# Performance work log

Hardware: AMD Instinct MI355X
Metric: run time of the kernel (lower is better)

The kernel has to match this reference:

```python
import jax, jax.numpy as jnp
import numpy as np

N_NODES = 100000
N_EDGES = 1000000
D_FEAT = 64
N_ETYPES = 8
TEMPERATURE = 1.0
EPS = 1e-8


def setup_inputs() -> dict:
    key = jax.random.key(0)
    k1, k2, k3, k4, k5, k6, k7 = jax.random.split(key, 7)
    feat = jax.random.normal(k1, (N_NODES, D_FEAT), dtype=jnp.float32)
    # xavier_normal-ish scale for params (exact init values don't matter for correctness testing)
    attn = jax.random.normal(k2, (1, D_FEAT), dtype=jnp.float32) * 0.1
    edge_weight = jax.random.normal(k3, (N_ETYPES, N_ETYPES), dtype=jnp.float32) * 0.5
    edge_weight_param = jax.random.normal(k4, (N_ETYPES, 1), dtype=jnp.float32) * 0.5
    src = jax.random.randint(k5, (N_EDGES,), 0, N_NODES, dtype=jnp.int32)
    dst = jax.random.randint(k6, (N_EDGES,), 0, N_NODES, dtype=jnp.int32)
    # e_feat is 1-based edge type (indexed as e_feat - 1 in the original module)
    e_feat = jax.random.randint(k7, (N_EDGES,), 1, N_ETYPES + 1, dtype=jnp.int32)
    return {"feat": feat, "attn": attn, "edge_weight": edge_weight,
            "edge_weight_param": edge_weight_param, "src": src, "dst": dst,
            "e_feat": e_feat}


def reference(feat, attn, edge_weight, edge_weight_param, src, dst, e_feat):
    N = feat.shape[0]
    # node mask: 1 where node feature vector is non-zero, else 0
    node_abs = jnp.sum(jnp.abs(feat), axis=-1, keepdims=True)          # [N,1]
    node_mask = jnp.where(node_abs == 0, 0.0, 1.0).astype(feat.dtype)  # [N,1]
    # per-node attention logit (feats_type == 6)
    nw = jnp.sum(feat * attn, axis=-1, keepdims=True)                  # [N,1]
    # per-edge-type weight: edge_weight @ edge_weight_param + 1
    ew_table = edge_weight @ edge_weight_param + 1.0                   # [T,1]
    ew = ew_table[e_feat - 1]                                          # [E,1]
    nw_exp = jnp.exp(nw / TEMPERATURE) * node_mask                     # [N,1]
    # message pass 1: copy_src(nw_exp) -> sum at dst (normalizer)
    msg_w = nw_exp[src]                                                # [E,1]
    nw_exp_sum = jax.ops.segment_sum(msg_w, dst, num_segments=N)       # [N,1]
    # apply_edges copy_src + per-edge-type scaling
    ew = msg_w * ew                                                    # [E,1]
    # message pass 2: u_mul_e(ft, ew) -> sum at dst
    ft = jax.ops.segment_sum(feat[src] * ew, dst, num_segments=N)      # [N,D]
    denom = jnp.where(nw_exp_sum < EPS, 1.0, nw_exp_sum)
    rst = ft / denom
    # keep original features for non-masked (nonzero) nodes
    rst = rst * (1.0 - node_mask) + feat * node_mask
    return rst


if __name__ == "__main__":
    out = reference(**setup_inputs())
    print(out.shape, out.dtype)
```

## Files before the change

### kernel.cpp

```cpp
#include <hip/hip_runtime.h>
#include <hip/hip_bf16.h>
#include <math.h>

#define D_FEAT 64
#define N_ETYPES 8
#define EPS_F 1e-8f

__global__ void node_kernel(const float* __restrict__ feat,
                            const float* __restrict__ attn,
                            float* __restrict__ out,
                            float* __restrict__ nw_exp,
                            float* __restrict__ nw_exp_sum,
                            int* __restrict__ mask,
                            int N) {
    int gid  = blockIdx.x * blockDim.x + threadIdx.x;
    int node = gid >> 4;
    int sub  = gid & 15;
    if (node >= N) return;

    const float4 f = ((const float4*)feat)[(size_t)node * 16 + sub];
    const float4 a = ((const float4*)attn)[sub];

    ((float4*)out)[(size_t)node * 16 + sub] = f;

    float abss = fabsf(f.x) + fabsf(f.y) + fabsf(f.z) + fabsf(f.w);
    float dot  = f.x * a.x + f.y * a.y + f.z * a.z + f.w * a.w;

    #pragma unroll
    for (int off = 1; off < 16; off <<= 1) {
        abss += __shfl_xor(abss, off);
        dot  += __shfl_xor(dot,  off);
    }

    if (sub == 0) {
        int m = (abss == 0.0f) ? 0 : 1;
        mask[node]       = m;
        nw_exp[node]     = m ? expf(dot) : 0.0f;
        nw_exp_sum[node] = 0.0f;
    }
}

__global__ void edge_kernel(const int* __restrict__ src,
                            const int* __restrict__ dst,
                            const int* __restrict__ e_feat,
                            const float* __restrict__ feat,
                            const float* __restrict__ nw_exp,
                            const int* __restrict__ mask,
                            const float* __restrict__ edge_weight,
                            const float* __restrict__ edge_weight_param,
                            float* __restrict__ out,
                            float* __restrict__ nw_exp_sum,
                            int E) {
    int e = blockIdx.x * blockDim.x + threadIdx.x;
    if (e >= E) return;
    int d = dst[e];
    if (mask[d] != 0) return;
    int s = src[e];
    float w = nw_exp[s];
    atomicAdd(&nw_exp_sum[d], w);
    int t = e_feat[e] - 1;
    float ewv = 1.0f;
    #pragma unroll
    for (int j = 0; j < N_ETYPES; ++j)
        ewv += edge_weight[t * N_ETYPES + j] * edge_weight_param[j];
    float scale = w * ewv;
    const float* fs = feat + (size_t)s * D_FEAT;
    float*       od = out  + (size_t)d * D_FEAT;
    #pragma unroll 4
    for (int k = 0; k < D_FEAT; ++k)
        atomicAdd(&od[k], fs[k] * scale);
}

__global__ void fixup_kernel(float* __restrict__ out,
                             const float* __restrict__ nw_exp_sum,
                             const int* __restrict__ mask,
                             int N) {
    int n = blockIdx.x * blockDim.x + threadIdx.x;
    if (n >= N || mask[n] != 0) return;
    float s = nw_exp_sum[n];
    float denom = (s < EPS_F) ? 1.0f : s;
    float* row = out + (size_t)n * D_FEAT;
    #pragma unroll 4
    for (int k = 0; k < D_FEAT; ++k)
        row[k] = row[k] / denom;
}

extern "C" void kernel_launch(void* const* d_in, const int* in_sizes, int n_in,
                              void* d_out, int out_size, void* d_ws, size_t ws_size,
                              hipStream_t stream) {
    const float* feat              = (const float*)d_in[0];
    const float* attn              = (const float*)d_in[1];
    const float* edge_weight       = (const float*)d_in[2];
    const float* edge_weight_param = (const float*)d_in[3];
    const int*   src               = (const int*)d_in[4];
    const int*   dst               = (const int*)d_in[5];
    const int*   e_feat            = (const int*)d_in[6];
    float*       out               = (float*)d_out;

    const int N = in_sizes[0] / D_FEAT;
    const int E = in_sizes[4];

    float* nw_exp     = (float*)d_ws;
    float* nw_exp_sum = nw_exp + N;
    int*   mask       = (int*)(nw_exp_sum + N);

    const int threadsA = 256;
    const int nodesPerBlock = threadsA / 16;
    node_kernel<<<(N + nodesPerBlock - 1) / nodesPerBlock, threadsA, 0, stream>>>(
        feat, attn, out, nw_exp, nw_exp_sum, mask, N);

    edge_kernel<<<(E + 255) / 256, 256, 0, stream>>>(
        src, dst, e_feat, feat, nw_exp, mask, edge_weight, edge_weight_param,
        out, nw_exp_sum, E);

    fixup_kernel<<<(N + 255) / 256, 256, 0, stream>>>(
        out, nw_exp_sum, mask, N);
}
```

Measured before the change: 98.55 us.

## Skip edge and fixup passes when no node has an all-zero feature row

The node kernel now raises a device flag whenever it finds an all-zero feature row. The edge and fixup kernels check that flag and exit at once when no such node exists, so in that case the 1M-edge scan with its dst/mask gathers is avoided. Per-node exp weight, running sum and mask are packed into one float4 side record, and feat/out copies use nontemporal loads and stores. The edge and fixup kernels switch to fixed-size grid-stride launches. The flag is never zeroed on the host, so the kernels rely on the workspace not already holding 1; a stale 1 only causes unneeded work, not a wrong result.

```diff
diff --git a/kernel.cpp b/kernel.cpp
--- a/kernel.cpp
+++ b/kernel.cpp
@@ -6,22 +6,23 @@
 #define N_ETYPES 8
 #define EPS_F 1e-8f
 
+typedef float v4f __attribute__((ext_vector_type(4)));
+
 __global__ void node_kernel(const float* __restrict__ feat,
                             const float* __restrict__ attn,
                             float* __restrict__ out,
-                            float* __restrict__ nw_exp,
-                            float* __restrict__ nw_exp_sum,
-                            int* __restrict__ mask,
+                            v4f* __restrict__ side,
+                            int* __restrict__ flag,
                             int N) {
     int gid  = blockIdx.x * blockDim.x + threadIdx.x;
     int node = gid >> 4;
     int sub  = gid & 15;
     if (node >= N) return;
 
-    const float4 f = ((const float4*)feat)[(size_t)node * 16 + sub];
-    const float4 a = ((const float4*)attn)[sub];
+    const v4f f = __builtin_nontemporal_load(((const v4f*)feat) + (size_t)node * 16 + sub);
+    const v4f a = ((const v4f*)attn)[sub];
 
-    ((float4*)out)[(size_t)node * 16 + sub] = f;
+    __builtin_nontemporal_store(f, ((v4f*)out) + (size_t)node * 16 + sub);
 
     float abss = fabsf(f.x) + fabsf(f.y) + fabsf(f.z) + fabsf(f.w);
     float dot  = f.x * a.x + f.y * a.y + f.z * a.z + f.w * a.w;
@@ -33,10 +34,14 @@
     }
 
     if (sub == 0) {
-        int m = (abss == 0.0f) ? 0 : 1;
-        mask[node]       = m;
-        nw_exp[node]     = m ? expf(dot) : 0.0f;
-        nw_exp_sum[node] = 0.0f;
+        float m = (abss == 0.0f) ? 0.0f : 1.0f;
+        v4f s;
+        s.x = (m != 0.0f) ? expf(dot) : 0.0f;
+        s.y = 0.0f;
+        s.z = m;
+        s.w = 0.0f;
+        side[node] = s;
+        if (m == 0.0f) *flag = 1;
     }
 }
 
@@ -44,45 +49,49 @@
                             const int* __restrict__ dst,
                             const int* __restrict__ e_feat,
                             const float* __restrict__ feat,
-                            const float* __restrict__ nw_exp,
-                            const int* __restrict__ mask,
+                            v4f* __restrict__ side,
                             const float* __restrict__ edge_weight,
                             const float* __restrict__ edge_weight_param,
+                            const int* __restrict__ flag,
                             float* __restrict__ out,
-                            float* __restrict__ nw_exp_sum,
                             int E) {
-    int e = blockIdx.x * blockDim.x + threadIdx.x;
-    if (e >= E) return;
-    int d = dst[e];
-    if (mask[d] != 0) return;
-    int s = src[e];
-    float w = nw_exp[s];
-    atomicAdd(&nw_exp_sum[d], w);
-    int t = e_feat[e] - 1;
-    float ewv = 1.0f;
-    #pragma unroll
-    for (int j = 0; j < N_ETYPES; ++j)
-        ewv += edge_weight[t * N_ETYPES + j] * edge_weight_param[j];
-    float scale = w * ewv;
-    const float* fs = feat + (size_t)s * D_FEAT;
-    float*       od = out  + (size_t)d * D_FEAT;
-    #pragma unroll 4
-    for (int k = 0; k < D_FEAT; ++k)
-        atomicAdd(&od[k], fs[k] * scale);
+    if (*flag != 1) return;
+    int stride = gridDim.x * blockDim.x;
+    for (int e = blockIdx.x * blockDim.x + threadIdx.x; e < E; e += stride) {
+        int d = dst[e];
+        if (side[d].z != 0.0f) continue;
+        int s = src[e];
+        float w = side[s].x;
+        atomicAdd(&((float*)&side[d])[1], w);
+        int t = e_feat[e] - 1;
+        float ewv = 1.0f;
+        #pragma unroll
+        for (int j = 0; j < N_ETYPES; ++j)
+            ewv += edge_weight[t * N_ETYPES + j] * edge_weight_param[j];
+        float scale = w * ewv;
+        const float* fs = feat + (size_t)s * D_FEAT;
+        float*       od = out  + (size_t)d * D_FEAT;
+        #pragma unroll 4
+        for (int k = 0; k < D_FEAT; ++k)
+            atomicAdd(&od[k], fs[k] * scale);
+    }
 }
 
 __global__ void fixup_kernel(float* __restrict__ out,
-                             const float* __restrict__ nw_exp_sum,
-                             const int* __restrict__ mask,
+                             const v4f* __restrict__ side,
+                             const int* __restrict__ flag,
                              int N) {
-    int n = blockIdx.x * blockDim.x + threadIdx.x;
-    if (n >= N || mask[n] != 0) return;
-    float s = nw_exp_sum[n];
-    float denom = (s < EPS_F) ? 1.0f : s;
-    float* row = out + (size_t)n * D_FEAT;
-    #pragma unroll 4
-    for (int k = 0; k < D_FEAT; ++k)
-        row[k] = row[k] / denom;
+    if (*flag != 1) return;
+    int stride = gridDim.x * blockDim.x;
+    for (int n = blockIdx.x * blockDim.x + threadIdx.x; n < N; n += stride) {
+        v4f s = side[n];
+        if (s.z != 0.0f) continue;
+        float denom = (s.y < EPS_F) ? 1.0f : s.y;
+        float* row = out + (size_t)n * D_FEAT;
+        #pragma unroll 4
+        for (int k = 0; k < D_FEAT; ++k)
+            row[k] = row[k] / denom;
+    }
 }
 
 extern "C" void kernel_launch(void* const* d_in, const int* in_sizes, int n_in,
@@ -100,19 +109,17 @@
     const int N = in_sizes[0] / D_FEAT;
     const int E = in_sizes[4];
 
-    float* nw_exp     = (float*)d_ws;
-    float* nw_exp_sum = nw_exp + N;
-    int*   mask       = (int*)(nw_exp_sum + N);
+    v4f* side = (v4f*)d_ws;
+    int* flag = (int*)(side + N);
 
     const int threadsA = 256;
     const int nodesPerBlock = threadsA / 16;
     node_kernel<<<(N + nodesPerBlock - 1) / nodesPerBlock, threadsA, 0, stream>>>(
-        feat, attn, out, nw_exp, nw_exp_sum, mask, N);
+        feat, attn, out, side, flag, N);
 
-    edge_kernel<<<(E + 255) / 256, 256, 0, stream>>>(
-        src, dst, e_feat, feat, nw_exp, mask, edge_weight, edge_weight_param,
-        out, nw_exp_sum, E);
+    edge_kernel<<<1024, 256, 0, stream>>>(
+        src, dst, e_feat, feat, side, edge_weight, edge_weight_param,
+        flag, out, E);
 
-    fixup_kernel<<<(N + 255) / 256, 256, 0, stream>>>(
-        out, nw_exp_sum, mask, N);
+    fixup_kernel<<<512, 256, 0, stream>>>(out, side, flag, N);
 }
```

Result: no change. 96.67 us (-1.9%).
